# Kernel optimization log

Measured on AMD Instinct MI355X. Metric: run time of the kernel, lower is better.

The kernel has to match this reference:

```python
import jax, jax.numpy as jnp
import numpy as np

B, L, H, E, V, Z, T = 256, 2, 1024, 256, 28, 1024, 512
SOS_IDX, EOS_IDX = 1, 0


def setup_inputs() -> dict:
    key = jax.random.key(0)
    ks = jax.random.split(key, 16)
    s = 0.05
    emb = s * jax.random.normal(ks[0], (V, E), jnp.float32)
    emb = emb.at[EOS_IDX].set(0.0)  # padding_idx=0
    return {
        "z": jax.random.normal(ks[1], (B, Z), jnp.float32),
        "emb": emb,
        "w_zh": s * jax.random.normal(ks[2], (L * H, Z), jnp.float32),
        "b_zh": jnp.zeros((L * H,), jnp.float32),
        "w_ih0": s * jax.random.normal(ks[3], (3 * H, E), jnp.float32),
        "w_hh0": s * jax.random.normal(ks[4], (3 * H, H), jnp.float32),
        "b_ih0": jnp.zeros((3 * H,), jnp.float32),
        "b_hh0": jnp.zeros((3 * H,), jnp.float32),
        "w_ih1": s * jax.random.normal(ks[5], (3 * H, H), jnp.float32),
        "w_hh1": s * jax.random.normal(ks[6], (3 * H, H), jnp.float32),
        "b_ih1": jnp.zeros((3 * H,), jnp.float32),
        "b_hh1": jnp.zeros((3 * H,), jnp.float32),
        "w_out": s * jax.random.normal(ks[7], (V, H), jnp.float32),
        "b_out": jnp.zeros((V,), jnp.float32),
    }


def _gru_cell(x, h, w_ih, w_hh, b_ih, b_hh):
    # PyTorch GRU cell math
    gi = x @ w_ih.T + b_ih          # [B, 3H]
    gh = h @ w_hh.T + b_hh          # [B, 3H]
    i_r, i_z, i_n = jnp.split(gi, 3, axis=-1)
    h_r, h_z, h_n = jnp.split(gh, 3, axis=-1)
    r = jax.nn.sigmoid(i_r + h_r)
    zg = jax.nn.sigmoid(i_z + h_z)
    n = jnp.tanh(i_n + r * h_n)
    return (1.0 - zg) * n + zg * h


def reference(z, emb, w_zh, b_zh, w_ih0, w_hh0, b_ih0, b_hh0,
              w_ih1, w_hh1, b_ih1, b_hh1, w_out, b_out):
    # init hidden from latent: (B, L*H) -> per-layer (B, H)
    h = jnp.tanh(z @ w_zh.T + b_zh).reshape(-1, L, H)
    h0, h1 = h[:, 0, :], h[:, 1, :]
    tok0 = jnp.full((z.shape[0],), SOS_IDX, jnp.int32)
    keys = jax.random.split(jax.random.key(42), T)

    def step(carry, k):
        tok, h0, h1 = carry
        x = emb[tok]                         # [B, E] embedding lookup
        h0n = _gru_cell(x, h0, w_ih0, w_hh0, b_ih0, b_hh0)
        h1n = _gru_cell(h0n, h1, w_ih1, w_hh1, b_ih1, b_hh1)
        logit = h1n @ w_out.T + b_out        # [B, V]
        tok_n = jax.random.categorical(k, logit)  # multinomial(softmax(logit))
        return (tok_n, h0n, h1n), (logit, tok_n)

    _, (logits, tokens) = jax.lax.scan(step, (tok0, h0, h1), keys)
    # [T, B, V] -> [B, T, V]; [T, B] -> [B, T]
    return logits.transpose(1, 0, 2), tokens.T
```

## Files before the change

### kernel.cpp

```cpp
#include <hip/hip_runtime.h>

#define BB 256
#define HH 1024
#define EE 256
#define VV 28
#define ZZ 1024
#define TT 512
#define G3 3072
#define NTHR 256
#define TOKBASE (BB * TT * VV)

#define BM 64
#define BN 64
#define KT 32

#define MMN 48
#define NBN 64

typedef float f4 __attribute__((ext_vector_type(4)));
typedef float f32x4 __attribute__((ext_vector_type(4)));
typedef _Float16 f16x8 __attribute__((ext_vector_type(8)));
typedef unsigned short u16x4 __attribute__((ext_vector_type(4)));
typedef unsigned short u16x8 __attribute__((ext_vector_type(8)));

#define RES_SCALE 512.0f
#define INV_RES (1.0f / 512.0f)

__device__ __align__(16) float g_h0[2][BB][HH];
__device__ __align__(16) float g_h1[2][BB][HH];
__device__ __align__(16) float g_gh0b[BB][G3];
__device__ __align__(16) float g_gh1b[BB][G3];
__device__ __align__(16) float g_gi1[BB][G3];
__device__ __align__(16) float g_P0[VV][G3];
__device__ __align__(16) unsigned short g_h0t[32][2][4][BB][8];
__device__ __align__(16) unsigned short g_h1t[32][2][4][BB][8];
__device__ __align__(16) unsigned short g_wt[3][NBN][32][2][4][MMN][8];

__device__ __forceinline__ uint2 tf2x32(unsigned k0, unsigned k1,
                                        unsigned x0, unsigned x1) {
  unsigned ks2 = k0 ^ k1 ^ 0x1BD11BDAu;
  unsigned ksl[3] = {k0, k1, ks2};
  x0 += k0; x1 += k1;
#pragma unroll
  for (int g = 0; g < 5; ++g) {
    const int r0 = (g & 1) ? 17 : 13;
    const int r1 = (g & 1) ? 29 : 15;
    const int r2 = (g & 1) ? 16 : 26;
    const int r3 = (g & 1) ? 24 : 6;
    x0 += x1; x1 = (x1 << r0) | (x1 >> (32 - r0)); x1 ^= x0;
    x0 += x1; x1 = (x1 << r1) | (x1 >> (32 - r1)); x1 ^= x0;
    x0 += x1; x1 = (x1 << r2) | (x1 >> (32 - r2)); x1 ^= x0;
    x0 += x1; x1 = (x1 << r3) | (x1 >> (32 - r3)); x1 ^= x0;
    x0 += ksl[(g + 1) % 3];
    x1 += ksl[(g + 2) % 3] + (unsigned)(g + 1);
  }
  return make_uint2(x0, x1);
}

__device__ __forceinline__ float sigf(float x) {
  return 1.0f / (1.0f + expf(-x));
}

__device__ __forceinline__ float gru_h(float i_r, float h_r, float i_z, float h_z,
                                       float i_n, float h_n, float hprev) {
  float r  = sigf(i_r + h_r);
  float zg = sigf(i_z + h_z);
  float n  = tanhf(i_n + r * h_n);
  return (1.0f - zg) * n + zg * hprev;
}

__device__ __forceinline__ void split2(float x, unsigned short& a,
                                       unsigned short& b) {
  _Float16 h1 = (_Float16)x;
  _Float16 h2 = (_Float16)((x - (float)h1) * RES_SCALE);
  a = __builtin_bit_cast(unsigned short, h1);
  b = __builtin_bit_cast(unsigned short, h2);
}

__device__ __forceinline__ void gload16(unsigned short* l, const unsigned short* g) {
  __builtin_amdgcn_global_load_lds(
      (const __attribute__((address_space(1))) unsigned int*)(g),
      (__attribute__((address_space(3))) unsigned int*)(l), 16, 0, 0);
}

__device__ __forceinline__ void gemm_unit(
    const float* __restrict__ At, int lda, int rows_valid,
    const float* __restrict__ Wt, int ldw,
    const float* __restrict__ bias,
    float* __restrict__ Ct, int ldc,
    int K, int mode,
    float (&As)[BM][KT + 4], float (&Ws)[KT][BN + 4]) {
  const int tid = threadIdx.x;
  const int tx = tid & 15, ty = tid >> 4;
  f4 acc0 = {0.f, 0.f, 0.f, 0.f};
  f4 acc1 = {0.f, 0.f, 0.f, 0.f};
  f4 acc2 = {0.f, 0.f, 0.f, 0.f};
  f4 acc3 = {0.f, 0.f, 0.f, 0.f};

  for (int kb = 0; kb < K; kb += KT) {
#pragma unroll
    for (int l = 0; l < 2; ++l) {
      int f = tid + l * NTHR;
      int r = f >> 3, kq = (f & 7) << 2;
      f4 v = {0.f, 0.f, 0.f, 0.f};
      if (r < rows_valid) v = *(const f4*)(At + r * lda + kb + kq);
      *(f4*)&As[r][kq] = v;
    }
#pragma unroll
    for (int l = 0; l < 2; ++l) {
      int f = tid + l * NTHR;
      int nr = f >> 3, kq = (f & 7) << 2;
      f4 v = *(const f4*)(Wt + nr * ldw + kb + kq);
      Ws[kq + 0][nr] = v[0];
      Ws[kq + 1][nr] = v[1];
      Ws[kq + 2][nr] = v[2];
      Ws[kq + 3][nr] = v[3];
    }
    __syncthreads();
#pragma unroll
    for (int kk = 0; kk < KT; kk += 4) {
      f4 a0 = *(const f4*)&As[(ty << 2) + 0][kk];
      f4 a1 = *(const f4*)&As[(ty << 2) + 1][kk];
      f4 a2 = *(const f4*)&As[(ty << 2) + 2][kk];
      f4 a3 = *(const f4*)&As[(ty << 2) + 3][kk];
      f4 b0 = *(const f4*)&Ws[kk + 0][tx << 2];
      f4 b1 = *(const f4*)&Ws[kk + 1][tx << 2];
      f4 b2 = *(const f4*)&Ws[kk + 2][tx << 2];
      f4 b3 = *(const f4*)&Ws[kk + 3][tx << 2];
      acc0 += b0 * a0[0]; acc0 += b1 * a0[1]; acc0 += b2 * a0[2]; acc0 += b3 * a0[3];
      acc1 += b0 * a1[0]; acc1 += b1 * a1[1]; acc1 += b2 * a1[2]; acc1 += b3 * a1[3];
      acc2 += b0 * a2[0]; acc2 += b1 * a2[1]; acc2 += b2 * a2[2]; acc2 += b3 * a2[3];
      acc3 += b0 * a3[0]; acc3 += b1 * a3[1]; acc3 += b2 * a3[2]; acc3 += b3 * a3[3];
    }
    __syncthreads();
  }

  f4 accs[4] = {acc0, acc1, acc2, acc3};
#pragma unroll
  for (int i = 0; i < 4; ++i) {
    int r = (ty << 2) + i;
    if (r < rows_valid) {
#pragma unroll
      for (int j = 0; j < 4; ++j) {
        int c = (tx << 2) + j;
        float v = accs[i][j] + bias[c];
        if (mode == 1) v = tanhf(v);
        Ct[r * ldc + c] = v;
      }
    }
  }
}

#define A_CH (2 * 4 * 256)
#define W_CH (2 * 4 * MMN)
#define BUFSZ ((A_CH + W_CH) * 8)

__device__ __forceinline__ void mm_tile(
    const unsigned short* __restrict__ At,
    const unsigned short* __restrict__ Wt,
    const float* __restrict__ bias,
    float* __restrict__ C,
    int n0, unsigned short* lds) {
  const int tid = threadIdx.x;
  const int wr = tid >> 6, lane = tid & 63;
  const int lr = lane & 15, lk8 = lane >> 4;

  f32x4 acc1[4][3] = {};
  f32x4 accR[4][3] = {};

  auto stage = [&](int buf, int ks) {
    unsigned short* lA = lds + buf * BUFSZ;
    unsigned short* lW = lA + A_CH * 8;
    const unsigned short* abase = At + (size_t)ks * (A_CH * 8);
#pragma unroll
    for (int r = 0; r < 8; ++r) {
      int j = r * NTHR + tid;
      gload16(lA + j * 8, abase + (size_t)j * 8);
    }
    const unsigned short* wbase = Wt + (size_t)ks * (W_CH * 8);
    gload16(lW + tid * 8, wbase + (size_t)tid * 8);
    if (tid < W_CH - NTHR) {
      int j = NTHR + tid;
      gload16(lW + j * 8, wbase + (size_t)j * 8);
    }
  };

  stage(0, 0);
  int cur = 0;
  for (int ks = 0; ks < HH / 32; ++ks) {
    __syncthreads();
    if (ks + 1 < HH / 32) stage(cur ^ 1, ks + 1);
    const unsigned short* lA = lds + cur * BUFSZ;
    const unsigned short* lW = lA + A_CH * 8;
    f16x8 a[4][2], b[3][2];
#pragma unroll
    for (int mi = 0; mi < 4; ++mi)
#pragma unroll
      for (int s = 0; s < 2; ++s)
        a[mi][s] = *(const f16x8*)(lA + (((s << 2) | lk8) * 256 + wr * 64 + mi * 16 + lr) * 8);
#pragma unroll
    for (int ni = 0; ni < 3; ++ni)
#pragma unroll
      for (int s = 0; s < 2; ++s)
        b[ni][s] = *(const f16x8*)(lW + (((s << 2) | lk8) * MMN + ni * 16 + lr) * 8);
#pragma unroll
    for (int mi = 0; mi < 4; ++mi)
#pragma unroll
      for (int ni = 0; ni < 3; ++ni) {
        acc1[mi][ni] = __builtin_amdgcn_mfma_f32_16x16x32_f16(a[mi][0], b[ni][0], acc1[mi][ni], 0, 0, 0);
        accR[mi][ni] = __builtin_amdgcn_mfma_f32_16x16x32_f16(a[mi][0], b[ni][1], accR[mi][ni], 0, 0, 0);
        accR[mi][ni] = __builtin_amdgcn_mfma_f32_16x16x32_f16(a[mi][1], b[ni][0], accR[mi][ni], 0, 0, 0);
      }
    cur ^= 1;
  }

#pragma unroll
  for (int mi = 0; mi < 4; ++mi) {
    int rowb = wr * 64 + mi * 16 + ((lane >> 4) << 2);
#pragma unroll
    for (int ni = 0; ni < 3; ++ni) {
      int col = n0 + ni * 16 + lr;
      float bv = bias[col];
#pragma unroll
      for (int r = 0; r < 4; ++r)
        C[(size_t)(rowb + r) * G3 + col] = acc1[mi][ni][r] + accR[mi][ni][r] * INV_RES + bv;
    }
  }
}

__device__ __forceinline__ void write_ht(unsigned short (*ht)[2][4][BB][8],
                                         int row, int k0,
                                         u16x4 o1, u16x4 o2) {
  const int ks = k0 >> 5, kk = (k0 >> 3) & 3, e0 = k0 & 7;
  *(u16x4*)&ht[ks][0][kk][row][e0] = o1;
  *(u16x4*)&ht[ks][1][kk][row][e0] = o2;
}

__global__ __launch_bounds__(NTHR) void k_setup1(
    const float* __restrict__ z, const float* __restrict__ w_zh,
    const float* __restrict__ b_zh, const float* __restrict__ emb,
    const float* __restrict__ w_ih0, const float* __restrict__ b_ih0) {
  __shared__ __align__(16) float As[BM][KT + 4];
  __shared__ __align__(16) float Ws[KT][BN + 4];
  const int bid = blockIdx.x;
  if (bid < 128) {
    int m0 = (bid >> 5) * BM;
    int n0 = (bid & 31) * BN;
    float* Cb;
    int col;
    if (n0 < HH) { Cb = &g_h0[1][0][0]; col = n0; }
    else         { Cb = &g_h1[1][0][0]; col = n0 - HH; }
    gemm_unit(z + m0 * ZZ, ZZ, BM, w_zh + n0 * ZZ, ZZ, b_zh + n0,
              Cb + m0 * HH + col, HH, ZZ, 1, As, Ws);
  } else {
    int n0 = (bid - 128) * BN;
    gemm_unit(emb, EE, VV, w_ih0 + n0 * EE, EE, b_ih0 + n0,
              &g_P0[0][0] + n0, G3, EE, 0, As, Ws);
  }
}

__global__ __launch_bounds__(NTHR) void k_splitw(
    const float* __restrict__ w_ih1, const float* __restrict__ w_hh0,
    const float* __restrict__ w_hh1) {
  unsigned u = blockIdx.x * NTHR + threadIdx.x;
  int row = u % MMN;
  unsigned v = u / MMN;
  int kk = v & 3, ks = (v >> 2) & 31;
  unsigned rem = v >> 7;
  int mat = rem / NBN, bn = rem % NBN;
  const float* src = (mat == 0) ? w_ih1 : (mat == 1) ? w_hh0 : w_hh1;
  const float* p = src + (size_t)(bn * MMN + row) * HH + ks * 32 + kk * 8;
  f4 v0 = *(const f4*)p;
  f4 v1 = *(const f4*)(p + 4);
  u16x8 o1, o2;
#pragma unroll
  for (int c = 0; c < 8; ++c) {
    float x = (c < 4) ? v0[c] : v1[c - 4];
    unsigned short a, b;
    split2(x, a, b);
    o1[c] = a; o2[c] = b;
  }
  *(u16x8*)&g_wt[mat][bn][ks][0][kk][row][0] = o1;
  *(u16x8*)&g_wt[mat][bn][ks][1][kk][row][0] = o2;
}

__global__ __launch_bounds__(NTHR) void k_splith() {
  unsigned e = blockIdx.x * NTHR + threadIdx.x;
  int mat = e >> 16, r = (e >> 8) & 255, k0 = (e & 255) << 2;
  const float* src = (mat == 0) ? &g_h0[1][0][0] : &g_h1[1][0][0];
  f4 v = *(const f4*)(src + (size_t)r * HH + k0);
  u16x4 o1, o2;
#pragma unroll
  for (int c = 0; c < 4; ++c) {
    unsigned short a, b;
    split2(v[c], a, b);
    o1[c] = a; o2[c] = b;
  }
  write_ht((mat == 0) ? g_h0t : g_h1t, r, k0, o1, o2);
}

__global__ __launch_bounds__(NTHR, 2) void k_mm_init(const float* __restrict__ b_hh0) {
  __shared__ __align__(16) unsigned short lds[2 * BUFSZ];
  int bn = blockIdx.x;
  mm_tile(&g_h0t[0][0][0][0][0], &g_wt[1][bn][0][0][0][0][0], b_hh0,
          &g_gh0b[0][0], bn * MMN, lds);
}

__global__ __launch_bounds__(NTHR) void k_gate0_init() {
  const int b = blockIdx.x, tid = threadIdx.x, j = tid << 2;
  const float* __restrict__ gi = g_P0[1];
  const float* __restrict__ gh = g_gh0b[b];
  f4 ir = *(const f4*)&gi[j];
  f4 iz = *(const f4*)&gi[j + HH];
  f4 in_ = *(const f4*)&gi[j + 2 * HH];
  f4 hr = *(const f4*)&gh[j];
  f4 hz = *(const f4*)&gh[j + HH];
  f4 hn = *(const f4*)&gh[j + 2 * HH];
  f4 hp = *(const f4*)&g_h0[1][b][j];
  f4 ho;
  u16x4 o1, o2;
#pragma unroll
  for (int c = 0; c < 4; ++c) {
    ho[c] = gru_h(ir[c], hr[c], iz[c], hz[c], in_[c], hn[c], hp[c]);
    unsigned short a, bb2;
    split2(ho[c], a, bb2);
    o1[c] = a; o2[c] = bb2;
  }
  *(f4*)&g_h0[0][b][j] = ho;
  write_ht(g_h0t, b, j, o1, o2);
}

__global__ __launch_bounds__(NTHR, 2) void k_mm(
    const float* __restrict__ b_ih1, const float* __restrict__ b_hh0,
    const float* __restrict__ b_hh1) {
  __shared__ __align__(16) unsigned short lds[2 * BUFSZ];
  const int bid = blockIdx.x;
  const int mat = bid >> 6, bn = bid & 63;
  const unsigned short* At = (mat == 2) ? &g_h1t[0][0][0][0][0] : &g_h0t[0][0][0][0][0];
  const unsigned short* Wt = &g_wt[mat][bn][0][0][0][0][0];
  const float* bias = (mat == 0) ? b_ih1 : (mat == 1) ? b_hh0 : b_hh1;
  float* C = (mat == 0) ? &g_gi1[0][0] : (mat == 1) ? &g_gh0b[0][0] : &g_gh1b[0][0];
  mm_tile(At, Wt, bias, C, bn * MMN, lds);
}

__global__ __launch_bounds__(NTHR) void k_fuse(
    int t, const float* __restrict__ w_out, const float* __restrict__ b_out,
    float* __restrict__ out) {
  __shared__ __align__(16) float s_h[HH];
  __shared__ float s_log[32];
  __shared__ float s_score[32];
  __shared__ int s_tok;
  const int b = blockIdx.x, tid = threadIdx.x, j = tid << 2;
  const int pw = t & 1, pr = pw ^ 1;

  {
    const float* __restrict__ gi = g_gi1[b];
    const float* __restrict__ gh = g_gh1b[b];
    f4 ir = *(const f4*)&gi[j];
    f4 iz = *(const f4*)&gi[j + HH];
    f4 in_ = *(const f4*)&gi[j + 2 * HH];
    f4 hr = *(const f4*)&gh[j];
    f4 hz = *(const f4*)&gh[j + HH];
    f4 hn = *(const f4*)&gh[j + 2 * HH];
    f4 hp = *(const f4*)&g_h1[pr][b][j];
    f4 ho;
    u16x4 o1, o2;
#pragma unroll
    for (int c = 0; c < 4; ++c) {
      ho[c] = gru_h(ir[c], hr[c], iz[c], hz[c], in_[c], hn[c], hp[c]);
      unsigned short a, bb2;
      split2(ho[c], a, bb2);
      o1[c] = a; o2[c] = bb2;
    }
    *(f4*)&g_h1[pw][b][j] = ho;
    *(f4*)&s_h[j] = ho;
    write_ht(g_h1t, b, j, o1, o2);
  }
  __syncthreads();

  {
    const int v = tid >> 3, ks = tid & 7;
    float part = 0.f;
    if (v < VV) {
      const float* __restrict__ wrow = w_out + v * HH + ks * 128;
      const float* __restrict__ hh = s_h + ks * 128;
#pragma unroll 8
      for (int i = 0; i < 128; i += 4) {
        f4 wv = *(const f4*)&wrow[i];
        f4 hv = *(const f4*)&hh[i];
        part += hv[0] * wv[0] + hv[1] * wv[1] + hv[2] * wv[2] + hv[3] * wv[3];
      }
    }
    part += __shfl_xor(part, 1);
    part += __shfl_xor(part, 2);
    part += __shfl_xor(part, 4);
    if (v < VV && ks == 0) s_log[v] = part;
  }
  __syncthreads();

  if (tid < VV) {
    float logit = s_log[tid] + b_out[tid];
    out[(size_t)b * (TT * VV) + (size_t)t * VV + tid] = logit;
    uint2 kt = tf2x32(0u, 42u, 0u, (unsigned)t);
    uint2 rr = tf2x32(kt.x, kt.y, 0u, (unsigned)(b * VV + tid));
    unsigned bits = rr.x ^ rr.y;
    float uf = __uint_as_float((bits >> 9) | 0x3f800000u) - 1.0f;
    if (uf <= 0.0f) uf = 1.17549435e-38f;
    s_score[tid] = logit - logf(-logf(uf));
  }
  __syncthreads();
  if (tid == 0) {
    float best = s_score[0];
    int bv = 0;
    for (int vv = 1; vv < VV; ++vv) {
      float s = s_score[vv];
      if (s > best) { best = s; bv = vv; }
    }
    s_tok = bv;
    out[TOKBASE + (size_t)b * TT + t] = (float)bv;
  }
  __syncthreads();

  {
    const int tok = s_tok;
    const float* __restrict__ gi = g_P0[tok];
    const float* __restrict__ gh = g_gh0b[b];
    f4 ir = *(const f4*)&gi[j];
    f4 iz = *(const f4*)&gi[j + HH];
    f4 in_ = *(const f4*)&gi[j + 2 * HH];
    f4 hr = *(const f4*)&gh[j];
    f4 hz = *(const f4*)&gh[j + HH];
    f4 hn = *(const f4*)&gh[j + 2 * HH];
    f4 hp = *(const f4*)&g_h0[pw][b][j];
    f4 ho;
    u16x4 o1, o2;
#pragma unroll
    for (int c = 0; c < 4; ++c) {
      ho[c] = gru_h(ir[c], hr[c], iz[c], hz[c], in_[c], hn[c], hp[c]);
      unsigned short a, bb2;
      split2(ho[c], a, bb2);
      o1[c] = a; o2[c] = bb2;
    }
    *(f4*)&g_h0[pr][b][j] = ho;
    write_ht(g_h0t, b, j, o1, o2);
  }
}

extern "C" void kernel_launch(void* const* d_in, const int* in_sizes, int n_in,
                              void* d_out, int out_size, void* d_ws, size_t ws_size,
                              hipStream_t stream) {
  (void)in_sizes; (void)n_in; (void)d_ws; (void)ws_size; (void)out_size;
  const float* z     = (const float*)d_in[0];
  const float* emb   = (const float*)d_in[1];
  const float* w_zh  = (const float*)d_in[2];
  const float* b_zh  = (const float*)d_in[3];
  const float* w_ih0 = (const float*)d_in[4];
  const float* w_hh0 = (const float*)d_in[5];
  const float* b_ih0 = (const float*)d_in[6];
  const float* b_hh0 = (const float*)d_in[7];
  const float* w_ih1 = (const float*)d_in[8];
  const float* w_hh1 = (const float*)d_in[9];
  const float* b_ih1 = (const float*)d_in[10];
  const float* b_hh1 = (const float*)d_in[11];
  const float* w_out = (const float*)d_in[12];
  const float* b_out = (const float*)d_in[13];
  float* out = (float*)d_out;

  k_setup1<<<dim3(176), dim3(NTHR), 0, stream>>>(z, w_zh, b_zh, emb, w_ih0, b_ih0);
  k_splitw<<<dim3(4608), dim3(NTHR), 0, stream>>>(w_ih1, w_hh0, w_hh1);
  k_splith<<<dim3(512), dim3(NTHR), 0, stream>>>();
  k_mm_init<<<dim3(64), dim3(NTHR), 0, stream>>>(b_hh0);
  k_gate0_init<<<dim3(BB), dim3(NTHR), 0, stream>>>();

  for (int t = 0; t < TT; ++t) {
    k_mm<<<dim3(192), dim3(NTHR), 0, stream>>>(b_ih1, b_hh0, b_hh1);
    k_fuse<<<dim3(BB), dim3(NTHR), 0, stream>>>(t, w_out, b_out, out);
  }
}
```

Before: 18.14 ms.

## Split recurrent matmul K dimension in two and reduce partials in fuse kernel

The per-step GEMM kernel now splits the K=1024 reduction into two halves, launching 384 blocks instead of 192 so more of the GPU's compute units are busy. Each half writes a partial result into a new g_part buffer, without bias. The fuse and init gate kernels sum the two partials and add the biases. The trade-off is extra global-memory writes and reads of the partial-sum buffers each step.

After: 16.73 ms. 7.8% less time.

```diff
diff --git a/kernel.cpp b/kernel.cpp
--- a/kernel.cpp
+++ b/kernel.cpp
@@ -28,9 +28,7 @@
 
 __device__ __align__(16) float g_h0[2][BB][HH];
 __device__ __align__(16) float g_h1[2][BB][HH];
-__device__ __align__(16) float g_gh0b[BB][G3];
-__device__ __align__(16) float g_gh1b[BB][G3];
-__device__ __align__(16) float g_gi1[BB][G3];
+__device__ __align__(16) float g_part[2][3][BB][G3];
 __device__ __align__(16) float g_P0[VV][G3];
 __device__ __align__(16) unsigned short g_h0t[32][2][4][BB][8];
 __device__ __align__(16) unsigned short g_h1t[32][2][4][BB][8];
@@ -154,13 +152,13 @@
 #define A_CH (2 * 4 * 256)
 #define W_CH (2 * 4 * MMN)
 #define BUFSZ ((A_CH + W_CH) * 8)
+#define KSH 16
 
 __device__ __forceinline__ void mm_tile(
     const unsigned short* __restrict__ At,
     const unsigned short* __restrict__ Wt,
-    const float* __restrict__ bias,
     float* __restrict__ C,
-    int n0, unsigned short* lds) {
+    int n0, int ks0, unsigned short* lds) {
   const int tid = threadIdx.x;
   const int wr = tid >> 6, lane = tid & 63;
   const int lr = lane & 15, lk8 = lane >> 4;
@@ -185,11 +183,11 @@
     }
   };
 
-  stage(0, 0);
+  stage(0, ks0);
   int cur = 0;
-  for (int ks = 0; ks < HH / 32; ++ks) {
+  for (int ks = ks0; ks < ks0 + KSH; ++ks) {
     __syncthreads();
-    if (ks + 1 < HH / 32) stage(cur ^ 1, ks + 1);
+    if (ks + 1 < ks0 + KSH) stage(cur ^ 1, ks + 1);
     const unsigned short* lA = lds + cur * BUFSZ;
     const unsigned short* lW = lA + A_CH * 8;
     f16x8 a[4][2], b[3][2];
@@ -220,10 +218,9 @@
 #pragma unroll
     for (int ni = 0; ni < 3; ++ni) {
       int col = n0 + ni * 16 + lr;
-      float bv = bias[col];
 #pragma unroll
       for (int r = 0; r < 4; ++r)
-        C[(size_t)(rowb + r) * G3 + col] = acc1[mi][ni][r] + accR[mi][ni][r] * INV_RES + bv;
+        C[(size_t)(rowb + r) * G3 + col] = acc1[mi][ni][r] + accR[mi][ni][r] * INV_RES;
     }
   }
 }
@@ -299,23 +296,25 @@
   write_ht((mat == 0) ? g_h0t : g_h1t, r, k0, o1, o2);
 }
 
-__global__ __launch_bounds__(NTHR, 2) void k_mm_init(const float* __restrict__ b_hh0) {
+__global__ __launch_bounds__(NTHR, 2) void k_mm_init() {
   __shared__ __align__(16) unsigned short lds[2 * BUFSZ];
-  int bn = blockIdx.x;
-  mm_tile(&g_h0t[0][0][0][0][0], &g_wt[1][bn][0][0][0][0][0], b_hh0,
-          &g_gh0b[0][0], bn * MMN, lds);
-}
-
-__global__ __launch_bounds__(NTHR) void k_gate0_init() {
+  int kh = blockIdx.x >> 6, bn = blockIdx.x & 63;
+  mm_tile(&g_h0t[0][0][0][0][0], &g_wt[1][bn][0][0][0][0][0],
+          &g_part[kh][1][0][0], bn * MMN, kh * KSH, lds);
+}
+
+__global__ __launch_bounds__(NTHR) void k_gate0_init(
+    const float* __restrict__ b_hh0) {
   const int b = blockIdx.x, tid = threadIdx.x, j = tid << 2;
   const float* __restrict__ gi = g_P0[1];
-  const float* __restrict__ gh = g_gh0b[b];
+  const float* __restrict__ ghA = g_part[0][1][b];
+  const float* __restrict__ ghB = g_part[1][1][b];
   f4 ir = *(const f4*)&gi[j];
   f4 iz = *(const f4*)&gi[j + HH];
   f4 in_ = *(const f4*)&gi[j + 2 * HH];
-  f4 hr = *(const f4*)&gh[j];
-  f4 hz = *(const f4*)&gh[j + HH];
-  f4 hn = *(const f4*)&gh[j + 2 * HH];
+  f4 hr = (*(const f4*)&ghA[j] + *(const f4*)&ghB[j]) + *(const f4*)&b_hh0[j];
+  f4 hz = (*(const f4*)&ghA[j + HH] + *(const f4*)&ghB[j + HH]) + *(const f4*)&b_hh0[j + HH];
+  f4 hn = (*(const f4*)&ghA[j + 2 * HH] + *(const f4*)&ghB[j + 2 * HH]) + *(const f4*)&b_hh0[j + 2 * HH];
   f4 hp = *(const f4*)&g_h0[1][b][j];
   f4 ho;
   u16x4 o1, o2;
@@ -330,22 +329,20 @@
   write_ht(g_h0t, b, j, o1, o2);
 }
 
-__global__ __launch_bounds__(NTHR, 2) void k_mm(
-    const float* __restrict__ b_ih1, const float* __restrict__ b_hh0,
-    const float* __restrict__ b_hh1) {
+__global__ __launch_bounds__(NTHR, 2) void k_mm() {
   __shared__ __align__(16) unsigned short lds[2 * BUFSZ];
   const int bid = blockIdx.x;
-  const int mat = bid >> 6, bn = bid & 63;
+  const int kh = bid / 192, r = bid % 192;
+  const int mat = r >> 6, bn = r & 63;
   const unsigned short* At = (mat == 2) ? &g_h1t[0][0][0][0][0] : &g_h0t[0][0][0][0][0];
   const unsigned short* Wt = &g_wt[mat][bn][0][0][0][0][0];
-  const float* bias = (mat == 0) ? b_ih1 : (mat == 1) ? b_hh0 : b_hh1;
-  float* C = (mat == 0) ? &g_gi1[0][0] : (mat == 1) ? &g_gh0b[0][0] : &g_gh1b[0][0];
-  mm_tile(At, Wt, bias, C, bn * MMN, lds);
+  mm_tile(At, Wt, &g_part[kh][mat][0][0], bn * MMN, kh * KSH, lds);
 }
 
 __global__ __launch_bounds__(NTHR) void k_fuse(
     int t, const float* __restrict__ w_out, const float* __restrict__ b_out,
-    float* __restrict__ out) {
+    const float* __restrict__ b_ih1, const float* __restrict__ b_hh0,
+    const float* __restrict__ b_hh1, float* __restrict__ out) {
   __shared__ __align__(16) float s_h[HH];
   __shared__ float s_log[32];
   __shared__ float s_score[32];
@@ -354,14 +351,16 @@
   const int pw = t & 1, pr = pw ^ 1;
 
   {
-    const float* __restrict__ gi = g_gi1[b];
-    const float* __restrict__ gh = g_gh1b[b];
-    f4 ir = *(const f4*)&gi[j];
-    f4 iz = *(const f4*)&gi[j + HH];
-    f4 in_ = *(const f4*)&gi[j + 2 * HH];
-    f4 hr = *(const f4*)&gh[j];
-    f4 hz = *(const f4*)&gh[j + HH];
-    f4 hn = *(const f4*)&gh[j + 2 * HH];
+    const float* __restrict__ giA = g_part[0][0][b];
+    const float* __restrict__ giB = g_part[1][0][b];
+    const float* __restrict__ ghA = g_part[0][2][b];
+    const float* __restrict__ ghB = g_part[1][2][b];
+    f4 ir = (*(const f4*)&giA[j] + *(const f4*)&giB[j]) + *(const f4*)&b_ih1[j];
+    f4 iz = (*(const f4*)&giA[j + HH] + *(const f4*)&giB[j + HH]) + *(const f4*)&b_ih1[j + HH];
+    f4 in_ = (*(const f4*)&giA[j + 2 * HH] + *(const f4*)&giB[j + 2 * HH]) + *(const f4*)&b_ih1[j + 2 * HH];
+    f4 hr = (*(const f4*)&ghA[j] + *(const f4*)&ghB[j]) + *(const f4*)&b_hh1[j];
+    f4 hz = (*(const f4*)&ghA[j + HH] + *(const f4*)&ghB[j + HH]) + *(const f4*)&b_hh1[j + HH];
+    f4 hn = (*(const f4*)&ghA[j + 2 * HH] + *(const f4*)&ghB[j + 2 * HH]) + *(const f4*)&b_hh1[j + 2 * HH];
     f4 hp = *(const f4*)&g_h1[pr][b][j];
     f4 ho;
     u16x4 o1, o2;
@@ -424,13 +423,14 @@
   {
     const int tok = s_tok;
     const float* __restrict__ gi = g_P0[tok];
-    const float* __restrict__ gh = g_gh0b[b];
+    const float* __restrict__ ghA = g_part[0][1][b];
+    const float* __restrict__ ghB = g_part[1][1][b];
     f4 ir = *(const f4*)&gi[j];
     f4 iz = *(const f4*)&gi[j + HH];
     f4 in_ = *(const f4*)&gi[j + 2 * HH];
-    f4 hr = *(const f4*)&gh[j];
-    f4 hz = *(const f4*)&gh[j + HH];
-    f4 hn = *(const f4*)&gh[j + 2 * HH];
+    f4 hr = (*(const f4*)&ghA[j] + *(const f4*)&ghB[j]) + *(const f4*)&b_hh0[j];
+    f4 hz = (*(const f4*)&ghA[j + HH] + *(const f4*)&ghB[j + HH]) + *(const f4*)&b_hh0[j + HH];
+    f4 hn = (*(const f4*)&ghA[j + 2 * HH] + *(const f4*)&ghB[j + 2 * HH]) + *(const f4*)&b_hh0[j + 2 * HH];
     f4 hp = *(const f4*)&g_h0[pw][b][j];
     f4 ho;
     u16x4 o1, o2;
@@ -469,11 +469,12 @@
   k_setup1<<<dim3(176), dim3(NTHR), 0, stream>>>(z, w_zh, b_zh, emb, w_ih0, b_ih0);
   k_splitw<<<dim3(4608), dim3(NTHR), 0, stream>>>(w_ih1, w_hh0, w_hh1);
   k_splith<<<dim3(512), dim3(NTHR), 0, stream>>>();
-  k_mm_init<<<dim3(64), dim3(NTHR), 0, stream>>>(b_hh0);
-  k_gate0_init<<<dim3(BB), dim3(NTHR), 0, stream>>>();
+  k_mm_init<<<dim3(128), dim3(NTHR), 0, stream>>>();
+  k_gate0_init<<<dim3(BB), dim3(NTHR), 0, stream>>>(b_hh0);
 
   for (int t = 0; t < TT; ++t) {
-    k_mm<<<dim3(192), dim3(NTHR), 0, stream>>>(b_ih1, b_hh0, b_hh1);
-    k_fuse<<<dim3(BB), dim3(NTHR), 0, stream>>>(t, w_out, b_out, out);
-  }
-}
+    k_mm<<<dim3(384), dim3(NTHR), 0, stream>>>();
+    k_fuse<<<dim3(BB), dim3(NTHR), 0, stream>>>(t, w_out, b_out, b_ih1, b_hh0,
+                                                b_hh1, out);
+  }
+}
```
